# Optimization experiments

Measured on AMD Instinct MI355X. Metric: run time of the kernel, lower is better.

The kernel has to match this reference:

```python
import jax, jax.numpy as jnp
import numpy as np

IN_FEATURES = 1024
N_CLASSES = 50257
CUTOFFS = [0, 5000, 20000, 50257]  # cluster boundaries (lows/highs)


def setup_inputs() -> dict:
    key = jax.random.key(0)
    ks = jax.random.split(key, 6)
    tokens = jax.random.randint(ks[0], (8, 4096), 0, N_CLASSES, dtype=jnp.int32)
    scale = 0.02
    head_emb = jax.random.normal(ks[1], (5000, IN_FEATURES), jnp.float32) * scale
    # tail cluster 0: hsz = 1024 // 2 = 512, osz = 20000 - 5000 = 15000
    tail0_emb = jax.random.normal(ks[2], (15000, 512), jnp.float32) * scale
    tail0_w = jax.random.normal(ks[3], (IN_FEATURES, 512), jnp.float32) * scale  # torch Linear weight (out, in)
    # tail cluster 1: hsz = 1024 // 4 = 256, osz = 50257 - 20000 = 30257
    tail1_emb = jax.random.normal(ks[4], (30257, 256), jnp.float32) * scale
    tail1_w = jax.random.normal(ks[5], (IN_FEATURES, 256), jnp.float32) * scale
    return {"tokens": tokens, "head_emb": head_emb, "tail0_emb": tail0_emb,
            "tail0_w": tail0_w, "tail1_emb": tail1_emb, "tail1_w": tail1_w}


def reference(tokens, head_emb, tail0_emb, tail0_w, tail1_emb, tail1_w):
    # AdaptiveInput forward (eval mode: Dropout = identity).
    # Each token id falls in exactly one cluster [low, high); lookup in that
    # cluster's table (shifted by low), project tails to in_features, scatter
    # back. We express gather+scatter as masked adds (clusters are disjoint).
    B, S = tokens.shape
    t = tokens.reshape(-1)  # [N]

    def cluster_out(low, high, table, w=None):
        mask = ((t >= low) & (t < high))[:, None]                 # [N, 1]
        idx = jnp.clip(t - low, 0, table.shape[0] - 1)            # in-range gather
        e = table[idx]                                            # [N, hsz]
        if w is not None:
            e = e @ w.T                                           # [N, in_features]
        return jnp.where(mask, e, jnp.zeros((), e.dtype))

    out = cluster_out(CUTOFFS[0], CUTOFFS[1], head_emb)
    out = out + cluster_out(CUTOFFS[1], CUTOFFS[2], tail0_emb, tail0_w)
    out = out + cluster_out(CUTOFFS[2], CUTOFFS[3], tail1_emb, tail1_w)
    return out.reshape(B, S, IN_FEATURES)
```

## Files before the change

kernel.cpp:

```cpp
#include <hip/hip_runtime.h>
#include <hip/hip_bf16.h>


typedef __attribute__((ext_vector_type(8))) short short8;
typedef __attribute__((ext_vector_type(4))) float f32x4;
typedef unsigned int u32;
typedef unsigned short u16;

__device__ __forceinline__ u32 pk2bf(float a, float b) {
    __hip_bfloat162 h = __float22bfloat162_rn(make_float2(a, b));
    union { __hip_bfloat162 h; u32 u; } c; c.h = h; return c.u;
}

__device__ __forceinline__ void glds16(const void* g, void* l) {
    __builtin_amdgcn_global_load_lds((const __attribute__((address_space(1))) u32*)g,
                                     (__attribute__((address_space(3))) u32*)l, 16, 0, 0);
}

__global__ __launch_bounds__(256) void ai_partition(const int* __restrict__ tokens, int n,
                                                    int* __restrict__ cnt,
                                                    int* __restrict__ l0, int* __restrict__ l1) {
    __shared__ int wcnt[4][3];
    __shared__ int wbase[4][3];
    int i = blockIdx.x * blockDim.x + threadIdx.x;
    int lane = threadIdx.x & 63, w = threadIdx.x >> 6;
    int t = (i < n) ? tokens[i] : -1;
    int c = (t < 0) ? 3 : (t >= 20000) ? 1 : (t >= 5000) ? 0 : 2;
    unsigned long long m0 = __ballot(c == 0);
    unsigned long long m1 = __ballot(c == 1);
    unsigned long long m2 = __ballot(c == 2);
    if (lane == 0) { wcnt[w][0] = __popcll(m0); wcnt[w][1] = __popcll(m1); wcnt[w][2] = __popcll(m2); }
    __syncthreads();
    if (threadIdx.x < 3) {
        int j = threadIdx.x;
        int s0 = wcnt[0][j], s1 = wcnt[1][j], s2 = wcnt[2][j], s3 = wcnt[3][j];
        int base = atomicAdd(&cnt[j], s0 + s1 + s2 + s3);
        wbase[0][j] = base; wbase[1][j] = base + s0;
        wbase[2][j] = base + s0 + s1; wbase[3][j] = base + s0 + s1 + s2;
    }
    __syncthreads();
    unsigned long long lt = (1ull << lane) - 1ull;
    if (c == 0)      l0[wbase[w][0] + __popcll(m0 & lt)] = i;
    else if (c == 1) l1[wbase[w][1] + __popcll(m1 & lt)] = i;
    else if (c == 2) l1[n - 1 - (wbase[w][2] + __popcll(m2 & lt))] = i;
}

__global__ __launch_bounds__(256) void ai_gather_cvt(
    const int* __restrict__ tokens,
    const int* __restrict__ l0, const int* __restrict__ l1,
    const int* __restrict__ cnt, int n,
    const float* __restrict__ e0f, const float* __restrict__ e1f,
    const float* __restrict__ w0f, const float* __restrict__ w1f,
    u16* __restrict__ a0p, u16* __restrict__ a1p,
    u16* __restrict__ wb0, u16* __restrict__ wb1)
{
    const int c0 = cnt[0], c1 = cnt[1];
    const int wItems = (1024 * 512 + 1024 * 256) / 8;
    const int i1 = wItems + n * 64;
    const int total = i1 + n * 32;
    for (int i = blockIdx.x * blockDim.x + threadIdx.x; i < total;
         i += gridDim.x * blockDim.x) {
        const float* s; u16* d; size_t so, dofs;
        if (i < wItems) {
            int j = i;
            if (j < 65536) { s = w0f; d = wb0; so = (size_t)j * 8; }
            else           { s = w1f; d = wb1; so = (size_t)(j - 65536) * 8; }
            dofs = so;
        } else if (i < i1) {
            int j = i - wItems;
            int m = j >> 6;
            if (m >= c0) continue;
            int k8 = j & 63;
            int er = tokens[l0[m]] - 5000;
            s = e0f; d = a0p;
            so = (size_t)er * 512 + k8 * 8;
            dofs = (size_t)m * 512 + k8 * 8;
        } else {
            int j = i - i1;
            int m = j >> 5;
            if (m >= c1) continue;
            int k8 = j & 31;
            int er = tokens[l1[m]] - 20000;
            s = e1f; d = a1p;
            so = (size_t)er * 256 + k8 * 8;
            dofs = (size_t)m * 256 + k8 * 8;
        }
        float4 a = *(const float4*)(s + so);
        float4 b = *(const float4*)(s + so + 4);
        uint4 q = { pk2bf(a.x, a.y), pk2bf(a.z, a.w), pk2bf(b.x, b.y), pk2bf(b.z, b.w) };
        *(uint4*)(d + dofs) = q;
    }
}

__global__ __launch_bounds__(256) void ai_head_copy(const int* __restrict__ tokens,
                                                    const int* __restrict__ l1, int n,
                                                    const int* __restrict__ cnt,
                                                    const float* __restrict__ emb,
                                                    float* __restrict__ out) {
    const int hc = cnt[2];
    for (int m = blockIdx.x; m < hc; m += gridDim.x) {
        int p = l1[n - 1 - m];
        int t = tokens[p];
        const float4* src = (const float4*)(emb + (size_t)t * 1024);
        float4* dst = (float4*)(out + (size_t)p * 1024);
        dst[threadIdx.x] = src[threadIdx.x];
    }
}

__global__ __launch_bounds__(256) void ai_tail_gemm(
    const int* __restrict__ l0, const int* __restrict__ l1,
    const int* __restrict__ cnt,
    const u16* __restrict__ a0p, const u16* __restrict__ a1p,
    const u16* __restrict__ wb0, const u16* __restrict__ wb1,
    float* __restrict__ out)
{
    constexpr int BK = 64;
    __shared__ __align__(16) u16 As[2][128 * BK];
    __shared__ __align__(16) u16 Bs[2][128 * BK];
    __shared__ int s_opos[128];

    const int z = blockIdx.z;
    const int K     = z ? 256 : 512;
    const int count = cnt[z];
    const int* list = z ? l1 : l0;
    const u16* ap   = z ? a1p : a0p;
    const u16* wb   = z ? wb1 : wb0;

    const int id = blockIdx.y * 8 + blockIdx.x;
    const int xcd = id & 7, q = id >> 3;
    const int m0 = (((q >> 3) << 3) | xcd) * 128;
    const int n0 = (q & 7) * 128;
    if (m0 >= count) return;
    const int tid = threadIdx.x;

    const int lane = tid & 63;
    const int wave = tid >> 6;
    const int wm = (wave >> 1) * 64;
    const int wn = (wave & 1) * 64;
    const int fr = lane & 15;
    const int fk = (lane >> 4) * 8;
    const int swzm = (fr & 7) << 4;

    const int rlc  = lane >> 3;
    const int c16s = (lane & 7) ^ rlc;

    const u16* aSrc[4];
    const u16* bSrc[4];
    #pragma unroll
    for (int i = 0; i < 4; i++) {
        int row = (wave * 4 + i) * 8 + rlc;
        int ar = m0 + row; if (ar >= count) ar = count - 1;
        aSrc[i] = ap + (size_t)ar * K + c16s * 8;
        bSrc[i] = wb + (size_t)(n0 + row) * K + c16s * 8;
    }

    auto issue = [&](int kt, int buf) {
        #pragma unroll
        for (int i = 0; i < 4; i++) {
            int chunk = wave * 4 + i;
            glds16(aSrc[i] + kt, &As[buf][chunk * 512]);
            glds16(bSrc[i] + kt, &Bs[buf][chunk * 512]);
        }
    };

    f32x4 acc[4][4];
    #pragma unroll
    for (int i = 0; i < 4; i++)
        #pragma unroll
        for (int j = 0; j < 4; j++)
            acc[i][j] = (f32x4){0.f, 0.f, 0.f, 0.f};

    issue(0, 0);

    if (tid < 128) {
        int m = m0 + tid;
        s_opos[tid] = (m < count) ? list[m] : -1;
    }

    auto compute = [&](int buf) {
        const char* Abase = (const char*)&As[buf][0];
        const char* Bbase = (const char*)&Bs[buf][0];
        #pragma unroll
        for (int kk = 0; kk < BK; kk += 32) {
            short8 af[4], bf[4];
            #pragma unroll
            for (int f = 0; f < 4; f++) {
                int ra = wm + f * 16 + fr;
                int rb = wn + f * 16 + fr;
                int cb = ((kk + fk) << 1) ^ swzm;
                af[f] = *(const short8*)(Abase + ra * 128 + cb);
                bf[f] = *(const short8*)(Bbase + rb * 128 + cb);
            }
            #pragma unroll
            for (int i = 0; i < 4; i++)
                #pragma unroll
                for (int j = 0; j < 4; j++)
                    acc[i][j] = __builtin_amdgcn_mfma_f32_16x16x32_bf16(af[i], bf[j], acc[i][j], 0, 0, 0);
        }
    };

    const int nt = K / BK;
    for (int t = 0; t < nt; t++) {
        const int cur = t & 1;
        if (t + 1 < nt) {
            issue((t + 1) * BK, cur ^ 1);
            asm volatile("s_waitcnt vmcnt(8)" ::: "memory");
        } else {
            asm volatile("s_waitcnt vmcnt(0)" ::: "memory");
        }
        __builtin_amdgcn_s_barrier();
        compute(cur);
        asm volatile("" ::: "memory");
        __builtin_amdgcn_s_barrier();
    }

    const int rbase = (lane >> 4) * 4;
    #pragma unroll
    for (int i = 0; i < 4; i++) {
        #pragma unroll
        for (int r = 0; r < 4; r++) {
            int ml = wm + i * 16 + rbase + r;
            if (m0 + ml < count) {
                float* orow = out + (size_t)s_opos[ml] * 1024 + n0 + wn + fr;
                orow[0]  = acc[i][0][r];
                orow[16] = acc[i][1][r];
                orow[32] = acc[i][2][r];
                orow[48] = acc[i][3][r];
            }
        }
    }
}

__global__ __launch_bounds__(256) void ai_naive(
    const int* __restrict__ tokens,
    const float* __restrict__ he,
    const float* __restrict__ e0, const float* __restrict__ w0,
    const float* __restrict__ e1, const float* __restrict__ w1,
    float* __restrict__ out)
{
    int p = blockIdx.x;
    int t = tokens[p];
    float* o = out + (size_t)p * 1024;
    if (t < 5000) {
        for (int j = threadIdx.x; j < 1024; j += 256) o[j] = he[(size_t)t * 1024 + j];
    } else if (t < 20000) {
        const float* e = e0 + (size_t)(t - 5000) * 512;
        for (int j = threadIdx.x; j < 1024; j += 256) {
            float s = 0.f;
            const float* wr = w0 + (size_t)j * 512;
            for (int k = 0; k < 512; k++) s += e[k] * wr[k];
            o[j] = s;
        }
    } else {
        const float* e = e1 + (size_t)(t - 20000) * 256;
        for (int j = threadIdx.x; j < 1024; j += 256) {
            float s = 0.f;
            const float* wr = w1 + (size_t)j * 256;
            for (int k = 0; k < 256; k++) s += e[k] * wr[k];
            o[j] = s;
        }
    }
}

extern "C" void kernel_launch(void* const* d_in, const int* in_sizes, int n_in,
                              void* d_out, int out_size, void* d_ws, size_t ws_size,
                              hipStream_t stream) {
    const int*   tokens   = (const int*)d_in[0];
    const float* head_emb = (const float*)d_in[1];
    const float* t0_emb   = (const float*)d_in[2];
    const float* t0_w     = (const float*)d_in[3];
    const float* t1_emb   = (const float*)d_in[4];
    const float* t1_w     = (const float*)d_in[5];
    float* out = (float*)d_out;
    const int N = in_sizes[0];
    const int nW0 = in_sizes[3];
    const int nW1 = in_sizes[5];

    int* cnt = (int*)d_ws;
    int* l0  = cnt + 16;
    int* l1  = l0 + N;
    size_t base_need = 64 + (size_t)2 * N * 4;
    size_t need = base_need + ((size_t)nW0 + nW1 + (size_t)N * 512 + (size_t)N * 256) * 2;
    if (ws_size < need) {
        ai_naive<<<N, 256, 0, stream>>>(tokens, head_emb, t0_emb, t0_w, t1_emb, t1_w, out);
        return;
    }
    u16* wb0 = (u16*)((char*)d_ws + base_need);
    u16* wb1 = wb0 + nW0;
    u16* a0p = wb1 + nW1;
    u16* a1p = a0p + (size_t)N * 512;

    hipMemsetAsync(cnt, 0, 64, stream);
    ai_partition<<<(N + 255) / 256, 256, 0, stream>>>(tokens, N, cnt, l0, l1);
    ai_gather_cvt<<<2048, 256, 0, stream>>>(tokens, l0, l1, cnt, N,
                                            t0_emb, t1_emb, t0_w, t1_w,
                                            a0p, a1p, wb0, wb1);
    ai_head_copy<<<1024, 256, 0, stream>>>(tokens, l1, N, cnt, head_emb, out);

    dim3 g(8, (N + 127) / 128, 2);
    ai_tail_gemm<<<g, 256, 0, stream>>>(l0, l1, cnt, a0p, a1p, wb0, wb1, out);
}
```

Before: 242.2 us.

## Fuse head copy into gather kernel and widen GEMM tile to 128x256 with 8 waves

The head-embedding copy kernel is folded into the gather/convert kernel, and that kernel's loop bounds now use the actual per-cluster counts instead of N, which removes one launch and the idle iterations. The tail GEMM moves to 512-thread blocks with 128x256 tiles, so each A tile is loaded once per 256 output columns. The wait count is adjusted to match, and s_setprio is raised around the MFMA compute. Larger LDS use and launch_bounds(512,2) may limit occupancy and raise register pressure.

```diff
diff --git a/kernel.cpp b/kernel.cpp
--- a/kernel.cpp
+++ b/kernel.cpp
@@ -51,16 +51,20 @@
     const int* __restrict__ cnt, int n,
     const float* __restrict__ e0f, const float* __restrict__ e1f,
     const float* __restrict__ w0f, const float* __restrict__ w1f,
+    const float* __restrict__ hef,
     u16* __restrict__ a0p, u16* __restrict__ a1p,
-    u16* __restrict__ wb0, u16* __restrict__ wb1)
+    u16* __restrict__ wb0, u16* __restrict__ wb1,
+    float* __restrict__ out)
 {
-    const int c0 = cnt[0], c1 = cnt[1];
+    const int c0 = cnt[0], c1 = cnt[1], hc = cnt[2];
     const int wItems = (1024 * 512 + 1024 * 256) / 8;
-    const int i1 = wItems + n * 64;
-    const int total = i1 + n * 32;
+    const int i1 = wItems + c0 * 64;
+    const int i2 = i1 + c1 * 32;
+    const int total = i2 + hc * 128;
     for (int i = blockIdx.x * blockDim.x + threadIdx.x; i < total;
          i += gridDim.x * blockDim.x) {
-        const float* s; u16* d; size_t so, dofs;
+        const float* s; size_t so;
+        u16* d; size_t dofs;
         if (i < wItems) {
             int j = i;
             if (j < 65536) { s = w0f; d = wb0; so = (size_t)j * 8; }
@@ -68,22 +72,28 @@
             dofs = so;
         } else if (i < i1) {
             int j = i - wItems;
-            int m = j >> 6;
-            if (m >= c0) continue;
-            int k8 = j & 63;
+            int m = j >> 6, k8 = j & 63;
             int er = tokens[l0[m]] - 5000;
             s = e0f; d = a0p;
             so = (size_t)er * 512 + k8 * 8;
             dofs = (size_t)m * 512 + k8 * 8;
-        } else {
+        } else if (i < i2) {
             int j = i - i1;
-            int m = j >> 5;
-            if (m >= c1) continue;
-            int k8 = j & 31;
+            int m = j >> 5, k8 = j & 31;
             int er = tokens[l1[m]] - 20000;
             s = e1f; d = a1p;
             so = (size_t)er * 256 + k8 * 8;
             dofs = (size_t)m * 256 + k8 * 8;
+        } else {
+            int j = i - i2;
+            int m = j >> 7, k8 = j & 127;
+            int p = l1[n - 1 - m];
+            int t = tokens[p];
+            const float4* src = (const float4*)(hef + (size_t)t * 1024 + k8 * 8);
+            float4* dst = (float4*)(out + (size_t)p * 1024 + k8 * 8);
+            dst[0] = src[0];
+            dst[1] = src[1];
+            continue;
         }
         float4 a = *(const float4*)(s + so);
         float4 b = *(const float4*)(s + so + 4);
@@ -92,22 +102,7 @@
     }
 }
 
-__global__ __launch_bounds__(256) void ai_head_copy(const int* __restrict__ tokens,
-                                                    const int* __restrict__ l1, int n,
-                                                    const int* __restrict__ cnt,
-                                                    const float* __restrict__ emb,
-                                                    float* __restrict__ out) {
-    const int hc = cnt[2];
-    for (int m = blockIdx.x; m < hc; m += gridDim.x) {
-        int p = l1[n - 1 - m];
-        int t = tokens[p];
-        const float4* src = (const float4*)(emb + (size_t)t * 1024);
-        float4* dst = (float4*)(out + (size_t)p * 1024);
-        dst[threadIdx.x] = src[threadIdx.x];
-    }
-}
-
-__global__ __launch_bounds__(256) void ai_tail_gemm(
+__global__ __launch_bounds__(512, 2) void ai_tail_gemm(
     const int* __restrict__ l0, const int* __restrict__ l1,
     const int* __restrict__ cnt,
     const u16* __restrict__ a0p, const u16* __restrict__ a1p,
@@ -116,7 +111,7 @@
 {
     constexpr int BK = 64;
     __shared__ __align__(16) u16 As[2][128 * BK];
-    __shared__ __align__(16) u16 Bs[2][128 * BK];
+    __shared__ __align__(16) u16 Bs[2][256 * BK];
     __shared__ int s_opos[128];
 
     const int z = blockIdx.z;
@@ -126,17 +121,16 @@
     const u16* ap   = z ? a1p : a0p;
     const u16* wb   = z ? wb1 : wb0;
 
-    const int id = blockIdx.y * 8 + blockIdx.x;
-    const int xcd = id & 7, q = id >> 3;
-    const int m0 = (((q >> 3) << 3) | xcd) * 128;
-    const int n0 = (q & 7) * 128;
+    const int id = blockIdx.y * 4 + blockIdx.x;
+    const int m0 = (((id >> 5) << 3) | (id & 7)) * 128;
+    const int n0 = ((id >> 3) & 3) * 256;
     if (m0 >= count) return;
     const int tid = threadIdx.x;
 
     const int lane = tid & 63;
     const int wave = tid >> 6;
-    const int wm = (wave >> 1) * 64;
-    const int wn = (wave & 1) * 64;
+    const int wm = (wave >> 2) * 64;
+    const int wn = (wave & 3) * 64;
     const int fr = lane & 15;
     const int fk = (lane >> 4) * 8;
     const int swzm = (fr & 7) << 4;
@@ -144,23 +138,27 @@
     const int rlc  = lane >> 3;
     const int c16s = (lane & 7) ^ rlc;
 
-    const u16* aSrc[4];
+    const u16* aSrc[2];
     const u16* bSrc[4];
+    #pragma unroll
+    for (int i = 0; i < 2; i++) {
+        int row = (wave * 2 + i) * 8 + rlc;
+        int ar = m0 + row; if (ar >= count) ar = count - 1;
+        aSrc[i] = ap + (size_t)ar * K + c16s * 8;
+    }
     #pragma unroll
     for (int i = 0; i < 4; i++) {
         int row = (wave * 4 + i) * 8 + rlc;
-        int ar = m0 + row; if (ar >= count) ar = count - 1;
-        aSrc[i] = ap + (size_t)ar * K + c16s * 8;
         bSrc[i] = wb + (size_t)(n0 + row) * K + c16s * 8;
     }
 
     auto issue = [&](int kt, int buf) {
         #pragma unroll
-        for (int i = 0; i < 4; i++) {
-            int chunk = wave * 4 + i;
-            glds16(aSrc[i] + kt, &As[buf][chunk * 512]);
-            glds16(bSrc[i] + kt, &Bs[buf][chunk * 512]);
-        }
+        for (int i = 0; i < 2; i++)
+            glds16(aSrc[i] + kt, &As[buf][(wave * 2 + i) * 512]);
+        #pragma unroll
+        for (int i = 0; i < 4; i++)
+            glds16(bSrc[i] + kt, &Bs[buf][(wave * 4 + i) * 512]);
     };
 
     f32x4 acc[4][4];
@@ -204,12 +202,14 @@
         const int cur = t & 1;
         if (t + 1 < nt) {
             issue((t + 1) * BK, cur ^ 1);
-            asm volatile("s_waitcnt vmcnt(8)" ::: "memory");
+            asm volatile("s_waitcnt vmcnt(6)" ::: "memory");
         } else {
             asm volatile("s_waitcnt vmcnt(0)" ::: "memory");
         }
         __builtin_amdgcn_s_barrier();
+        __builtin_amdgcn_s_setprio(1);
         compute(cur);
+        __builtin_amdgcn_s_setprio(0);
         asm volatile("" ::: "memory");
         __builtin_amdgcn_s_barrier();
     }
@@ -293,10 +293,9 @@
     hipMemsetAsync(cnt, 0, 64, stream);
     ai_partition<<<(N + 255) / 256, 256, 0, stream>>>(tokens, N, cnt, l0, l1);
     ai_gather_cvt<<<2048, 256, 0, stream>>>(tokens, l0, l1, cnt, N,
-                                            t0_emb, t1_emb, t0_w, t1_w,
-                                            a0p, a1p, wb0, wb1);
-    ai_head_copy<<<1024, 256, 0, stream>>>(tokens, l1, N, cnt, head_emb, out);
-
-    dim3 g(8, (N + 127) / 128, 2);
-    ai_tail_gemm<<<g, 256, 0, stream>>>(l0, l1, cnt, a0p, a1p, wb0, wb1, out);
-}
+                                            t0_emb, t1_emb, t0_w, t1_w, head_emb,
+                                            a0p, a1p, wb0, wb1, out);
+
+    dim3 g(4, (N + 127) / 128, 2);
+    ai_tail_gemm<<<g, 512, 0, stream>>>(l0, l1, cnt, a0p, a1p, wb0, wb1, out);
+}
```

Measured after the change: 241.7 us. Within noise of the previous version (-0.2%).
